# Kernel optimization log

Hardware: AMD Instinct MI355X
Metric: run time of the kernel (lower is better)

Reference implementation:

```python
import jax, jax.numpy as jnp
import numpy as np

B, N, D, H = 8, 1024, 512, 8
HD = D // H
SCALE = 1.0 / np.sqrt(HD).astype(np.float32)


def setup_inputs() -> dict:
    key = jax.random.key(0)
    ks = jax.random.split(key, 7)
    x = jax.random.normal(ks[0], (B, N, D), dtype=jnp.float32)
    U = jax.random.normal(ks[1], (N, N), dtype=jnp.float32)
    attn_mask = jax.random.uniform(ks[2], (B, 1, 1, N), dtype=jnp.float32)
    # learned params: qkv projection D->3D and output projection D->D (with bias)
    w_qkv = jax.random.normal(ks[3], (D, 3 * D), dtype=jnp.float32) / np.sqrt(D).astype(np.float32)
    b_qkv = jnp.zeros((3 * D,), dtype=jnp.float32)
    w_out = jax.random.normal(ks[4], (D, D), dtype=jnp.float32) / np.sqrt(D).astype(np.float32)
    b_out = jnp.zeros((D,), dtype=jnp.float32)
    return {"x": x, "U": U, "attn_mask": attn_mask,
            "w_qkv": w_qkv, "b_qkv": b_qkv, "w_out": w_out, "b_out": b_out}


def reference(x, U, attn_mask, w_qkv, b_qkv, w_out, b_out):
    # QKV projection (QuantIdentity layers are identity in math; key_value = x)
    qkv = x @ w_qkv + b_qkv                       # [B, N, 3D]
    q, k, v = jnp.split(qkv, 3, axis=-1)          # each [B, N, D]

    def split_heads(t):
        return t.reshape(B, N, H, HD).transpose(0, 2, 1, 3)  # [B, H, N, HD]

    qh, kh, vh = split_heads(q), split_heads(k), split_heads(v)
    scores = jnp.einsum('bhqd,bhkd->bhqk', qh, kh) * SCALE   # [B, H, N, N]
    scores = scores + U[None, None, :, :]                    # additive interaction bias
    scores = scores + attn_mask                              # [B,1,1,N] broadcast add
    attn = jax.nn.softmax(scores, axis=-1)
    ctx = jnp.einsum('bhqk,bhkd->bhqd', attn, vh)            # [B, H, N, HD]
    ctx = ctx.transpose(0, 2, 1, 3).reshape(B, N, D)         # merge heads
    out = ctx @ w_out + b_out                                # [B, N, D]
    return out
```

## Files before the change

kernel.cpp:

```cpp
#include <hip/hip_runtime.h>

#define DEV __device__ __forceinline__

typedef __attribute__((ext_vector_type(8))) __bf16 bf16x8;
typedef __attribute__((ext_vector_type(4))) __bf16 bf16x4;
typedef __attribute__((ext_vector_type(4))) float f32x4;
typedef __attribute__((ext_vector_type(4))) float float4v;

typedef __attribute__((address_space(1))) const void ga_void;
typedef __attribute__((address_space(3))) void la_void;

constexpr float LOG2E = 1.44269504089f;
constexpr float ATT_SCALE2 = 0.125f * 1.44269504089f;

#if __has_builtin(__builtin_amdgcn_exp2f)
#define EXP2(x) __builtin_amdgcn_exp2f(x)
#else
#define EXP2(x) exp2f(x)
#endif

DEV void gload16(const void* g, void* l) {
  __builtin_amdgcn_global_load_lds((ga_void*)g, (la_void*)l, 16, 0, 0);
}

DEV f32x4 mfma_bf16(bf16x8 a, bf16x8 b, f32x4 c) {
  return __builtin_amdgcn_mfma_f32_16x16x32_bf16(a, b, c, 0, 0, 0);
}

__global__ __launch_bounds__(256) void cast_x_kernel(
    const float* __restrict__ in, __bf16* __restrict__ out, int n4) {
  int i = blockIdx.x * blockDim.x + threadIdx.x;
  int stride = gridDim.x * blockDim.x;
  for (; i < n4; i += stride) {
    float4v v = ((const float4v*)in)[i];
    bf16x4 o;
    o[0] = (__bf16)v[0]; o[1] = (__bf16)v[1];
    o[2] = (__bf16)v[2]; o[3] = (__bf16)v[3];
    ((bf16x4*)out)[i] = o;
  }
}

__global__ __launch_bounds__(256) void transpose_cast_kernel(
    const float* __restrict__ in, __bf16* __restrict__ out, int K, int Nc) {
  __shared__ float tile[32][33];
  int bx = blockIdx.x * 32;
  int by = blockIdx.y * 32;
  int tx = threadIdx.x, ty = threadIdx.y;
#pragma unroll
  for (int i = ty; i < 32; i += 8)
    tile[i][tx] = in[(size_t)(by + i) * Nc + bx + tx];
  __syncthreads();
#pragma unroll
  for (int i = ty; i < 32; i += 8)
    out[(size_t)(bx + i) * K + by + tx] = (__bf16)tile[tx][i];
}

__global__ __launch_bounds__(256) void gemm_qkv_kernel(
    const __bf16* __restrict__ A, const __bf16* __restrict__ Bt,
    const float* __restrict__ bias,
    __bf16* __restrict__ Qo, __bf16* __restrict__ Ko, __bf16* __restrict__ Vto) {
  __shared__ __align__(16) __bf16 As[2][128 * 32];
  __shared__ __align__(16) __bf16 Bs[2][128 * 32];
  const int tid = threadIdx.x;
  const int lane = tid & 63;
  const int w = tid >> 6;
  const int lr = lane & 15, lg = lane >> 4;
  const int m0 = blockIdx.x * 128, n0 = blockIdx.y * 128;
  const int wr = w >> 1, wc = w & 1;

  f32x4 acc[4][4] = {};

  auto stage = [&](int buf, int kt) {
#pragma unroll
    for (int cc = 0; cc < 2; ++cc) {
      int c = w * 2 + cc;
      int row = c * 16 + (lane >> 2);
      int slot = (lane & 3) ^ ((row >> 1) & 3);
      gload16(A + (size_t)(m0 + row) * 512 + kt * 32 + slot * 8, &As[buf][c * 512]);
      gload16(Bt + (size_t)(n0 + row) * 512 + kt * 32 + slot * 8, &Bs[buf][c * 512]);
    }
  };

  stage(0, 0);
  __syncthreads();
  for (int kt = 0; kt < 16; ++kt) {
    int cur = kt & 1;
    if (kt < 15) stage(cur ^ 1, kt + 1);
    bf16x8 av[4], bv[4];
#pragma unroll
    for (int i = 0; i < 4; ++i) {
      int row = wr * 64 + i * 16 + lr;
      av[i] = *(const bf16x8*)&As[cur][row * 32 + ((lg ^ ((row >> 1) & 3)) * 8)];
    }
#pragma unroll
    for (int j = 0; j < 4; ++j) {
      int row = wc * 64 + j * 16 + lr;
      bv[j] = *(const bf16x8*)&Bs[cur][row * 32 + ((lg ^ ((row >> 1) & 3)) * 8)];
    }
#pragma unroll
    for (int i = 0; i < 4; ++i)
#pragma unroll
      for (int j = 0; j < 4; ++j)
        acc[i][j] = mfma_bf16(av[i], bv[j], acc[i][j]);
    __syncthreads();
  }

  const int sec = n0 >> 9;
#pragma unroll
  for (int j = 0; j < 4; ++j) {
    int n = n0 + wc * 64 + j * 16 + lr;
    float bsv = bias[n];
    int nn = n & 511;
    int h = nn >> 6, d = nn & 63;
#pragma unroll
    for (int i = 0; i < 4; ++i) {
#pragma unroll
      for (int r = 0; r < 4; ++r) {
        int m = m0 + wr * 64 + i * 16 + lg * 4 + r;
        int b = m >> 10, nr = m & 1023;
        float v = acc[i][j][r] + bsv;
        if (sec == 0)
          Qo[(((size_t)(b * 8 + h)) * 1024 + nr) * 64 + d] = (__bf16)v;
        else if (sec == 1)
          Ko[(((size_t)(b * 8 + h)) * 1024 + nr) * 64 + d] = (__bf16)v;
        else
          Vto[(((size_t)(b * 8 + h)) * 64 + d) * 1024 + nr] = (__bf16)v;
      }
    }
  }
}

__global__ __launch_bounds__(256) void gemm_out_kernel(
    const __bf16* __restrict__ A, const __bf16* __restrict__ Bt,
    const float* __restrict__ bias, float* __restrict__ out) {
  __shared__ __align__(16) __bf16 As[2][128 * 32];
  __shared__ __align__(16) __bf16 Bs[2][128 * 32];
  const int tid = threadIdx.x;
  const int lane = tid & 63;
  const int w = tid >> 6;
  const int lr = lane & 15, lg = lane >> 4;
  const int m0 = blockIdx.x * 128, n0 = blockIdx.y * 128;
  const int wr = w >> 1, wc = w & 1;

  f32x4 acc[4][4] = {};

  auto stage = [&](int buf, int kt) {
#pragma unroll
    for (int cc = 0; cc < 2; ++cc) {
      int c = w * 2 + cc;
      int row = c * 16 + (lane >> 2);
      int slot = (lane & 3) ^ ((row >> 1) & 3);
      gload16(A + (size_t)(m0 + row) * 512 + kt * 32 + slot * 8, &As[buf][c * 512]);
      gload16(Bt + (size_t)(n0 + row) * 512 + kt * 32 + slot * 8, &Bs[buf][c * 512]);
    }
  };

  stage(0, 0);
  __syncthreads();
  for (int kt = 0; kt < 16; ++kt) {
    int cur = kt & 1;
    if (kt < 15) stage(cur ^ 1, kt + 1);
    bf16x8 av[4], bv[4];
#pragma unroll
    for (int i = 0; i < 4; ++i) {
      int row = wr * 64 + i * 16 + lr;
      av[i] = *(const bf16x8*)&As[cur][row * 32 + ((lg ^ ((row >> 1) & 3)) * 8)];
    }
#pragma unroll
    for (int j = 0; j < 4; ++j) {
      int row = wc * 64 + j * 16 + lr;
      bv[j] = *(const bf16x8*)&Bs[cur][row * 32 + ((lg ^ ((row >> 1) & 3)) * 8)];
    }
#pragma unroll
    for (int i = 0; i < 4; ++i)
#pragma unroll
      for (int j = 0; j < 4; ++j)
        acc[i][j] = mfma_bf16(av[i], bv[j], acc[i][j]);
    __syncthreads();
  }

#pragma unroll
  for (int j = 0; j < 4; ++j) {
    int n = n0 + wc * 64 + j * 16 + lr;
    float bsv = bias[n];
#pragma unroll
    for (int i = 0; i < 4; ++i) {
#pragma unroll
      for (int r = 0; r < 4; ++r) {
        int m = m0 + wr * 64 + i * 16 + lg * 4 + r;
        out[(size_t)m * 512 + n] = acc[i][j][r] + bsv;
      }
    }
  }
}

__global__ __launch_bounds__(256, 4) void attn_kernel(
    const __bf16* __restrict__ Qh, const __bf16* __restrict__ Kh,
    const __bf16* __restrict__ Vth, const float* __restrict__ U,
    const float* __restrict__ mask, __bf16* __restrict__ ctx) {
  __shared__ __align__(16) __bf16 Ks[2][64 * 64];
  __shared__ __align__(16) __bf16 Vs[2][64 * 64];
  __shared__ __align__(16) __bf16 Ps[4][16 * 64];
  const int tid = threadIdx.x;
  const int lane = tid & 63;
  const int w = tid >> 6;
  const int lr = lane & 15, lg = lane >> 4;
  const int bh = blockIdx.x, qb = blockIdx.y;
  const int b = bh >> 3, h = bh & 7;

  bf16x8 qf[2];
  {
    const __bf16* qp = Qh + ((size_t)bh * 1024 + qb * 64 + w * 16 + lr) * 64;
    qf[0] = *(const bf16x8*)(qp + lg * 8);
    qf[1] = *(const bf16x8*)(qp + 32 + lg * 8);
  }

  f32x4 acc_o[4] = {};
  float m_run[4], l_run[4];
#pragma unroll
  for (int r = 0; r < 4; ++r) { m_run[r] = -3e38f; l_run[r] = 0.f; }

  auto stageKV = [&](int buf, int kb) {
#pragma unroll
    for (int i = 0; i < 2; ++i) {
      int gid = i * 256 + tid;
      int row = gid >> 3, slot = gid & 7;
      int sg = slot ^ (row & 7);
      gload16(Kh + ((size_t)bh * 1024 + kb * 64 + row) * 64 + sg * 8,
              &Ks[buf][(i * 256 + w * 64) * 8]);
      gload16(Vth + ((size_t)bh * 64 + row) * 1024 + kb * 64 + sg * 8,
              &Vs[buf][(i * 256 + w * 64) * 8]);
    }
  };

  const float* Urow = U + (size_t)(qb * 64 + w * 16) * 1024;
  const float* mrow = mask + b * 1024;
  __bf16* pw = &Ps[w][0];

  stageKV(0, 0);
  __builtin_amdgcn_sched_barrier(0);
  asm volatile("s_waitcnt vmcnt(0)" ::: "memory");
  __builtin_amdgcn_s_barrier();
  asm volatile("" ::: "memory");
  __builtin_amdgcn_sched_barrier(0);

  for (int kb = 0; kb < 16; ++kb) {
    const int cur = kb & 1;
    if (kb < 15) stageKV(cur ^ 1, kb + 1);
    __builtin_amdgcn_sched_barrier(0);

    float uc[4][4], mc[4];
#pragma unroll
    for (int t = 0; t < 4; ++t) {
      mc[t] = mrow[kb * 64 + t * 16 + lr];
#pragma unroll
      for (int r = 0; r < 4; ++r)
        uc[t][r] = Urow[(size_t)(lg * 4 + r) * 1024 + kb * 64 + t * 16 + lr];
    }

    f32x4 sv[4];
    __builtin_amdgcn_s_setprio(1);
#pragma unroll
    for (int t = 0; t < 4; ++t) {
      int krow = t * 16 + lr;
      const __bf16* kp = &Ks[cur][krow * 64];
      int sw = krow & 7;
      bf16x8 k0 = *(const bf16x8*)(kp + ((lg ^ sw) * 8));
      bf16x8 k1 = *(const bf16x8*)(kp + (((4 + lg) ^ sw) * 8));
      f32x4 z = {0.f, 0.f, 0.f, 0.f};
      z = mfma_bf16(qf[0], k0, z);
      z = mfma_bf16(qf[1], k1, z);
      sv[t] = z;
    }
    __builtin_amdgcn_s_setprio(0);

    float mk2[4];
#pragma unroll
    for (int t = 0; t < 4; ++t) mk2[t] = mc[t] * LOG2E;
    float sval[4][4];
#pragma unroll
    for (int t = 0; t < 4; ++t)
#pragma unroll
      for (int r = 0; r < 4; ++r)
        sval[t][r] = fmaf(uc[t][r], LOG2E, fmaf(sv[t][r], ATT_SCALE2, mk2[t]));

    float mx[4];
#pragma unroll
    for (int r = 0; r < 4; ++r) {
      float m = fmaxf(fmaxf(sval[0][r], sval[1][r]), fmaxf(sval[2][r], sval[3][r]));
      m = fmaxf(m, __shfl_xor(m, 1));
      m = fmaxf(m, __shfl_xor(m, 2));
      m = fmaxf(m, __shfl_xor(m, 4));
      m = fmaxf(m, __shfl_xor(m, 8));
      mx[r] = m;
    }
    bool grow = (mx[0] > m_run[0] + 8.f) || (mx[1] > m_run[1] + 8.f) ||
                (mx[2] > m_run[2] + 8.f) || (mx[3] > m_run[3] + 8.f);
    if (__any(grow)) {
#pragma unroll
      for (int r = 0; r < 4; ++r) {
        float mnew = fmaxf(m_run[r], mx[r]);
        float f = EXP2(m_run[r] - mnew);
        m_run[r] = mnew;
        l_run[r] *= f;
#pragma unroll
        for (int t = 0; t < 4; ++t) acc_o[t][r] *= f;
      }
    }
    float pval[4][4];
#pragma unroll
    for (int r = 0; r < 4; ++r) {
      float ps = 0.f;
#pragma unroll
      for (int t = 0; t < 4; ++t) {
        float p = EXP2(sval[t][r] - m_run[r]);
        pval[t][r] = p;
        ps += p;
      }
      ps += __shfl_xor(ps, 1);
      ps += __shfl_xor(ps, 2);
      ps += __shfl_xor(ps, 4);
      ps += __shfl_xor(ps, 8);
      l_run[r] += ps;
    }

#pragma unroll
    for (int t = 0; t < 4; ++t)
#pragma unroll
      for (int r = 0; r < 4; ++r) {
        int q = lg * 4 + r;
        int k = t * 16 + lr;
        pw[q * 64 + (k ^ ((q & 7) << 3))] = (__bf16)pval[t][r];
      }

    bf16x8 pa0, pa1;
    {
      const __bf16* pp = &pw[lr * 64];
      int sw = lr & 7;
      pa0 = *(const bf16x8*)(pp + ((lg ^ sw) * 8));
      pa1 = *(const bf16x8*)(pp + (((4 + lg) ^ sw) * 8));
    }
    __builtin_amdgcn_s_setprio(1);
#pragma unroll
    for (int t = 0; t < 4; ++t) {
      int vrow = t * 16 + lr;
      const __bf16* vp = &Vs[cur][vrow * 64];
      int sw = vrow & 7;
      bf16x8 v0 = *(const bf16x8*)(vp + ((lg ^ sw) * 8));
      bf16x8 v1 = *(const bf16x8*)(vp + (((4 + lg) ^ sw) * 8));
      acc_o[t] = mfma_bf16(pa0, v0, acc_o[t]);
      acc_o[t] = mfma_bf16(pa1, v1, acc_o[t]);
    }
    __builtin_amdgcn_s_setprio(0);

    if (kb < 15) {
      __builtin_amdgcn_sched_barrier(0);
      asm volatile("s_waitcnt vmcnt(0)" ::: "memory");
      __builtin_amdgcn_s_barrier();
      asm volatile("" ::: "memory");
      __builtin_amdgcn_sched_barrier(0);
    }
  }

  float inv[4];
#pragma unroll
  for (int r = 0; r < 4; ++r) inv[r] = 1.0f / l_run[r];
#pragma unroll
  for (int t = 0; t < 4; ++t)
#pragma unroll
    for (int r = 0; r < 4; ++r) {
      int qrow = qb * 64 + w * 16 + lg * 4 + r;
      int d = t * 16 + lr;
      ctx[((size_t)(b * 1024 + qrow)) * 512 + h * 64 + d] = (__bf16)(acc_o[t][r] * inv[r]);
    }
}

extern "C" void kernel_launch(void* const* d_in, const int* in_sizes, int n_in,
                              void* d_out, int out_size, void* d_ws, size_t ws_size,
                              hipStream_t stream) {
  (void)in_sizes; (void)n_in; (void)out_size; (void)ws_size;
  const float* x     = (const float*)d_in[0];
  const float* U     = (const float*)d_in[1];
  const float* mask  = (const float*)d_in[2];
  const float* w_qkv = (const float*)d_in[3];
  const float* b_qkv = (const float*)d_in[4];
  const float* w_out = (const float*)d_in[5];
  const float* b_out = (const float*)d_in[6];
  float* out = (float*)d_out;

  char* p = (char*)d_ws;
  __bf16* xb    = (__bf16*)p; p += (size_t)8192 * 512 * 2;
  __bf16* wqkvT = (__bf16*)p; p += (size_t)1536 * 512 * 2;
  __bf16* woutT = (__bf16*)p; p += (size_t)512 * 512 * 2;
  __bf16* Qh    = (__bf16*)p; p += (size_t)64 * 1024 * 64 * 2;
  __bf16* Kh    = (__bf16*)p; p += (size_t)64 * 1024 * 64 * 2;
  __bf16* Vth   = (__bf16*)p; p += (size_t)64 * 64 * 1024 * 2;
  __bf16* ctx   = (__bf16*)p; p += (size_t)8192 * 512 * 2;

  hipLaunchKernelGGL(cast_x_kernel, dim3(2048), dim3(256), 0, stream,
                     x, xb, 8192 * 512 / 4);
  hipLaunchKernelGGL(transpose_cast_kernel, dim3(48, 16), dim3(32, 8), 0, stream,
                     w_qkv, wqkvT, 512, 1536);
  hipLaunchKernelGGL(transpose_cast_kernel, dim3(16, 16), dim3(32, 8), 0, stream,
                     w_out, woutT, 512, 512);
  hipLaunchKernelGGL(gemm_qkv_kernel, dim3(64, 12), dim3(256), 0, stream,
                     xb, wqkvT, b_qkv, Qh, Kh, Vth);
  hipLaunchKernelGGL(attn_kernel, dim3(64, 16), dim3(256), 0, stream,
                     Qh, Kh, Vth, U, mask, ctx);
  hipLaunchKernelGGL(gemm_out_kernel, dim3(64, 4), dim3(256), 0, stream,
                     ctx, woutT, b_out, out);
}
```

Measured before the change: 106.5 us.

## Transpose attention MFMA operands for row-per-lane softmax; shrink output GEMM tiles

The attention kernel swaps the MFMA operand order so each lane owns a single query row across four consecutive keys. This lets U and mask load as contiguous float4 vectors, turns the row max and sum into two cross-lane shuffles, and writes P and ctx as packed bf16x4 stores. Separately, the output GEMM moves from 128x128 to 64x64 tiles, giving 1024 blocks instead of 256 so more CUs stay busy. The cost is lower per-block data reuse in the GEMM.

Result: no change. 105.0 us (-1.3%).

```diff
diff --git a/kernel.cpp b/kernel.cpp
--- a/kernel.cpp
+++ b/kernel.cpp
@@ -133,26 +133,21 @@
 __global__ __launch_bounds__(256) void gemm_out_kernel(
     const __bf16* __restrict__ A, const __bf16* __restrict__ Bt,
     const float* __restrict__ bias, float* __restrict__ out) {
-  __shared__ __align__(16) __bf16 As[2][128 * 32];
-  __shared__ __align__(16) __bf16 Bs[2][128 * 32];
+  __shared__ __align__(16) __bf16 As[2][64 * 32];
+  __shared__ __align__(16) __bf16 Bs[2][64 * 32];
   const int tid = threadIdx.x;
   const int lane = tid & 63;
   const int w = tid >> 6;
   const int lr = lane & 15, lg = lane >> 4;
-  const int m0 = blockIdx.x * 128, n0 = blockIdx.y * 128;
-  const int wr = w >> 1, wc = w & 1;
-
-  f32x4 acc[4][4] = {};
+  const int m0 = blockIdx.x * 64, n0 = blockIdx.y * 64;
+
+  f32x4 acc[4] = {};
 
   auto stage = [&](int buf, int kt) {
-#pragma unroll
-    for (int cc = 0; cc < 2; ++cc) {
-      int c = w * 2 + cc;
-      int row = c * 16 + (lane >> 2);
-      int slot = (lane & 3) ^ ((row >> 1) & 3);
-      gload16(A + (size_t)(m0 + row) * 512 + kt * 32 + slot * 8, &As[buf][c * 512]);
-      gload16(Bt + (size_t)(n0 + row) * 512 + kt * 32 + slot * 8, &Bs[buf][c * 512]);
-    }
+    int row = tid >> 2;
+    int sg = (tid & 3) ^ ((row >> 1) & 3);
+    gload16(A + (size_t)(m0 + row) * 512 + kt * 32 + sg * 8, &As[buf][tid * 8]);
+    gload16(Bt + (size_t)(n0 + row) * 512 + kt * 32 + sg * 8, &Bs[buf][tid * 8]);
   };
 
   stage(0, 0);
@@ -160,36 +155,25 @@
   for (int kt = 0; kt < 16; ++kt) {
     int cur = kt & 1;
     if (kt < 15) stage(cur ^ 1, kt + 1);
-    bf16x8 av[4], bv[4];
-#pragma unroll
-    for (int i = 0; i < 4; ++i) {
-      int row = wr * 64 + i * 16 + lr;
-      av[i] = *(const bf16x8*)&As[cur][row * 32 + ((lg ^ ((row >> 1) & 3)) * 8)];
-    }
+    int arow = w * 16 + lr;
+    bf16x8 av = *(const bf16x8*)&As[cur][arow * 32 + ((lg ^ ((arow >> 1) & 3)) * 8)];
 #pragma unroll
     for (int j = 0; j < 4; ++j) {
-      int row = wc * 64 + j * 16 + lr;
-      bv[j] = *(const bf16x8*)&Bs[cur][row * 32 + ((lg ^ ((row >> 1) & 3)) * 8)];
-    }
-#pragma unroll
-    for (int i = 0; i < 4; ++i)
-#pragma unroll
-      for (int j = 0; j < 4; ++j)
-        acc[i][j] = mfma_bf16(av[i], bv[j], acc[i][j]);
+      int brow = j * 16 + lr;
+      bf16x8 bv = *(const bf16x8*)&Bs[cur][brow * 32 + ((lg ^ ((brow >> 1) & 3)) * 8)];
+      acc[j] = mfma_bf16(av, bv, acc[j]);
+    }
     __syncthreads();
   }
 
 #pragma unroll
   for (int j = 0; j < 4; ++j) {
-    int n = n0 + wc * 64 + j * 16 + lr;
+    int n = n0 + j * 16 + lr;
     float bsv = bias[n];
 #pragma unroll
-    for (int i = 0; i < 4; ++i) {
-#pragma unroll
-      for (int r = 0; r < 4; ++r) {
-        int m = m0 + wr * 64 + i * 16 + lg * 4 + r;
-        out[(size_t)m * 512 + n] = acc[i][j][r] + bsv;
-      }
+    for (int r = 0; r < 4; ++r) {
+      int m = m0 + w * 16 + lg * 4 + r;
+      out[(size_t)m * 512 + n] = acc[j][r] + bsv;
     }
   }
 }
@@ -208,17 +192,17 @@
   const int bh = blockIdx.x, qb = blockIdx.y;
   const int b = bh >> 3, h = bh & 7;
 
+  const int qrow = qb * 64 + w * 16 + lr;
+
   bf16x8 qf[2];
   {
-    const __bf16* qp = Qh + ((size_t)bh * 1024 + qb * 64 + w * 16 + lr) * 64;
+    const __bf16* qp = Qh + ((size_t)bh * 1024 + qrow) * 64;
     qf[0] = *(const bf16x8*)(qp + lg * 8);
     qf[1] = *(const bf16x8*)(qp + 32 + lg * 8);
   }
 
   f32x4 acc_o[4] = {};
-  float m_run[4], l_run[4];
-#pragma unroll
-  for (int r = 0; r < 4; ++r) { m_run[r] = -3e38f; l_run[r] = 0.f; }
+  float m_run = -3e38f, l_run = 0.f;
 
   auto stageKV = [&](int buf, int kb) {
 #pragma unroll
@@ -233,8 +217,8 @@
     }
   };
 
-  const float* Urow = U + (size_t)(qb * 64 + w * 16) * 1024;
-  const float* mrow = mask + b * 1024;
+  const float* Uq = U + (size_t)qrow * 1024 + lg * 4;
+  const float* mq = mask + b * 1024 + lg * 4;
   __bf16* pw = &Ps[w][0];
 
   stageKV(0, 0);
@@ -249,13 +233,11 @@
     if (kb < 15) stageKV(cur ^ 1, kb + 1);
     __builtin_amdgcn_sched_barrier(0);
 
-    float uc[4][4], mc[4];
+    float4v uc[4], mc[4];
 #pragma unroll
     for (int t = 0; t < 4; ++t) {
-      mc[t] = mrow[kb * 64 + t * 16 + lr];
-#pragma unroll
-      for (int r = 0; r < 4; ++r)
-        uc[t][r] = Urow[(size_t)(lg * 4 + r) * 1024 + kb * 64 + t * 16 + lr];
+      uc[t] = *(const float4v*)(Uq + kb * 64 + t * 16);
+      mc[t] = *(const float4v*)(mq + kb * 64 + t * 16);
     }
 
     f32x4 sv[4];
@@ -268,70 +250,56 @@
       bf16x8 k0 = *(const bf16x8*)(kp + ((lg ^ sw) * 8));
       bf16x8 k1 = *(const bf16x8*)(kp + (((4 + lg) ^ sw) * 8));
       f32x4 z = {0.f, 0.f, 0.f, 0.f};
-      z = mfma_bf16(qf[0], k0, z);
-      z = mfma_bf16(qf[1], k1, z);
+      z = mfma_bf16(k0, qf[0], z);
+      z = mfma_bf16(k1, qf[1], z);
       sv[t] = z;
     }
     __builtin_amdgcn_s_setprio(0);
 
-    float mk2[4];
-#pragma unroll
-    for (int t = 0; t < 4; ++t) mk2[t] = mc[t] * LOG2E;
-    float sval[4][4];
 #pragma unroll
     for (int t = 0; t < 4; ++t)
 #pragma unroll
       for (int r = 0; r < 4; ++r)
-        sval[t][r] = fmaf(uc[t][r], LOG2E, fmaf(sv[t][r], ATT_SCALE2, mk2[t]));
-
-    float mx[4];
-#pragma unroll
-    for (int r = 0; r < 4; ++r) {
-      float m = fmaxf(fmaxf(sval[0][r], sval[1][r]), fmaxf(sval[2][r], sval[3][r]));
-      m = fmaxf(m, __shfl_xor(m, 1));
-      m = fmaxf(m, __shfl_xor(m, 2));
-      m = fmaxf(m, __shfl_xor(m, 4));
-      m = fmaxf(m, __shfl_xor(m, 8));
-      mx[r] = m;
-    }
-    bool grow = (mx[0] > m_run[0] + 8.f) || (mx[1] > m_run[1] + 8.f) ||
-                (mx[2] > m_run[2] + 8.f) || (mx[3] > m_run[3] + 8.f);
-    if (__any(grow)) {
+        sv[t][r] = fmaf(uc[t][r], LOG2E, fmaf(sv[t][r], ATT_SCALE2, mc[t][r] * LOG2E));
+
+    float mx = sv[0][0];
+#pragma unroll
+    for (int t = 0; t < 4; ++t)
+#pragma unroll
+      for (int r = 0; r < 4; ++r) mx = fmaxf(mx, sv[t][r]);
+    mx = fmaxf(mx, __shfl_xor(mx, 16));
+    mx = fmaxf(mx, __shfl_xor(mx, 32));
+
+    if (__any(mx > m_run + 8.f)) {
+      float mnew = fmaxf(m_run, mx);
+      float f = EXP2(m_run - mnew);
+      m_run = mnew;
+      l_run *= f;
+#pragma unroll
+      for (int t = 0; t < 4; ++t) acc_o[t] *= f;
+    }
+
+    float ps = 0.f;
+#pragma unroll
+    for (int t = 0; t < 4; ++t)
 #pragma unroll
       for (int r = 0; r < 4; ++r) {
-        float mnew = fmaxf(m_run[r], mx[r]);
-        float f = EXP2(m_run[r] - mnew);
-        m_run[r] = mnew;
-        l_run[r] *= f;
-#pragma unroll
-        for (int t = 0; t < 4; ++t) acc_o[t][r] *= f;
-      }
-    }
-    float pval[4][4];
-#pragma unroll
-    for (int r = 0; r < 4; ++r) {
-      float ps = 0.f;
-#pragma unroll
-      for (int t = 0; t < 4; ++t) {
-        float p = EXP2(sval[t][r] - m_run[r]);
-        pval[t][r] = p;
+        float p = EXP2(sv[t][r] - m_run);
+        sv[t][r] = p;
         ps += p;
       }
-      ps += __shfl_xor(ps, 1);
-      ps += __shfl_xor(ps, 2);
-      ps += __shfl_xor(ps, 4);
-      ps += __shfl_xor(ps, 8);
-      l_run[r] += ps;
-    }
-
-#pragma unroll
-    for (int t = 0; t < 4; ++t)
-#pragma unroll
-      for (int r = 0; r < 4; ++r) {
-        int q = lg * 4 + r;
-        int k = t * 16 + lr;
-        pw[q * 64 + (k ^ ((q & 7) << 3))] = (__bf16)pval[t][r];
-      }
+    ps += __shfl_xor(ps, 16);
+    ps += __shfl_xor(ps, 32);
+    l_run += ps;
+
+#pragma unroll
+    for (int t = 0; t < 4; ++t) {
+      bf16x4 pk;
+      pk[0] = (__bf16)sv[t][0]; pk[1] = (__bf16)sv[t][1];
+      pk[2] = (__bf16)sv[t][2]; pk[3] = (__bf16)sv[t][3];
+      int k0 = t * 16 + lg * 4;
+      *(bf16x4*)&pw[lr * 64 + (k0 ^ ((lr & 7) << 3))] = pk;
+    }
 
     bf16x8 pa0, pa1;
     {
@@ -348,8 +316,8 @@
       int sw = vrow & 7;
       bf16x8 v0 = *(const bf16x8*)(vp + ((lg ^ sw) * 8));
       bf16x8 v1 = *(const bf16x8*)(vp + (((4 + lg) ^ sw) * 8));
-      acc_o[t] = mfma_bf16(pa0, v0, acc_o[t]);
-      acc_o[t] = mfma_bf16(pa1, v1, acc_o[t]);
+      acc_o[t] = mfma_bf16(v0, pa0, acc_o[t]);
+      acc_o[t] = mfma_bf16(v1, pa1, acc_o[t]);
     }
     __builtin_amdgcn_s_setprio(0);
 
@@ -362,17 +330,15 @@
     }
   }
 
-  float inv[4];
-#pragma unroll
-  for (int r = 0; r < 4; ++r) inv[r] = 1.0f / l_run[r];
-#pragma unroll
-  for (int t = 0; t < 4; ++t)
-#pragma unroll
-    for (int r = 0; r < 4; ++r) {
-      int qrow = qb * 64 + w * 16 + lg * 4 + r;
-      int d = t * 16 + lr;
-      ctx[((size_t)(b * 1024 + qrow)) * 512 + h * 64 + d] = (__bf16)(acc_o[t][r] * inv[r]);
-    }
+  float inv = 1.0f / l_run;
+  __bf16* cp = ctx + ((size_t)(b * 1024 + qrow)) * 512 + h * 64 + lg * 4;
+#pragma unroll
+  for (int t = 0; t < 4; ++t) {
+    bf16x4 ov;
+    ov[0] = (__bf16)(acc_o[t][0] * inv); ov[1] = (__bf16)(acc_o[t][1] * inv);
+    ov[2] = (__bf16)(acc_o[t][2] * inv); ov[3] = (__bf16)(acc_o[t][3] * inv);
+    *(bf16x4*)(cp + t * 16) = ov;
+  }
 }
 
 extern "C" void kernel_launch(void* const* d_in, const int* in_sizes, int n_in,
@@ -407,6 +373,6 @@
                      xb, wqkvT, b_qkv, Qh, Kh, Vth);
   hipLaunchKernelGGL(attn_kernel, dim3(64, 16), dim3(256), 0, stream,
                      Qh, Kh, Vth, U, mask, ctx);
-  hipLaunchKernelGGL(gemm_out_kernel, dim3(64, 4), dim3(256), 0, stream,
+  hipLaunchKernelGGL(gemm_out_kernel, dim3(128, 8), dim3(256), 0, stream,
                      ctx, woutT, b_out, out);
 }
```
